# Kernel tuning notes

Measured on AMD Instinct MI355X. Metric: run time of the kernel, lower is better.

Reference implementation:

```python
import jax, jax.numpy as jnp
import numpy as np
import math

B, L, S, T = 16, 128, 128, 128
QDIM, FDIM, HID, ODIM = 512, 512, 512, 512

def setup_inputs() -> dict:
    key = jax.random.key(0)
    ks = jax.random.split(key, 9)
    sc = 0.02
    return {
        "query": jax.random.normal(ks[0], (B, L, QDIM), dtype=jnp.float32),
        "src": jax.random.normal(ks[1], (B, S, FDIM), dtype=jnp.float32),
        "trg": jax.random.normal(ks[2], (B, T, FDIM), dtype=jnp.float32),
        "Wq": jax.random.normal(ks[3], (QDIM, HID), dtype=jnp.float32) * sc,
        "bq": jnp.zeros((HID,), dtype=jnp.float32),
        "Ws": jax.random.normal(ks[4], (FDIM, HID), dtype=jnp.float32) * sc,
        "bs": jnp.zeros((HID,), dtype=jnp.float32),
        "Wo": jax.random.normal(ks[5], (FDIM * 2 + QDIM, ODIM), dtype=jnp.float32) * sc,
        "bo": jnp.zeros((ODIM,), dtype=jnp.float32),
    }

def reference(query, src, trg, Wq, bq, Ws, bs, Wo, bo):
    b, l, _ = query.shape
    s = src.shape[1]
    t = trg.shape[1]
    q = query @ Wq + bq            # [b,l,h]
    s_key = src @ Ws + bs          # [b,s,h]  (src_linear == trg_linear, shared weights)
    t_key = trg @ Ws + bs          # [b,t,h]
    # trilinear scores: [b,l,s,t]
    weight = jnp.einsum('blk,bsk,btk->blst', q, s_key, t_key) / math.sqrt(HID)
    weight = jax.nn.softmax(weight.reshape(b, l, s * t), axis=-1).reshape(b, l, s, t)
    s_ctx = jnp.einsum('blst,bsf->blf', weight, src)
    t_ctx = jnp.einsum('blst,btf->blf', weight, trg)
    x = jnp.concatenate((query, s_ctx, t_ctx), axis=-1)
    return x @ Wo + bo
```

## Files before the change

### kernel.cpp

```cpp
#include <hip/hip_runtime.h>
#include <hip/hip_bf16.h>

typedef __attribute__((ext_vector_type(8))) short short8;
typedef __attribute__((ext_vector_type(4))) short short4v;
typedef __attribute__((ext_vector_type(4))) float f32x4;
typedef __attribute__((ext_vector_type(8))) _Float16 half8;

#define DEVINL static __device__ __forceinline__

constexpr float SCORE_SCALE = 0.063758977414048896f;

typedef const __attribute__((address_space(1))) void gv_t;
typedef __attribute__((address_space(3))) void lv_t;
DEVINL void gload16(const void* g, void* l) {
  __builtin_amdgcn_global_load_lds((gv_t*)g, (lv_t*)l, 16, 0, 0);
}

#define SWZ_ADD(v, pat)                                                    \
  v += __int_as_float(__builtin_amdgcn_ds_swizzle(__float_as_int(v), pat))

template <int M, int N>
DEVINL void gemm16(const _Float16* A, const _Float16* B, int K, int lda, int ldb,
                   _Float16* ldsA, _Float16* ldsB, f32x4 acc[M / 32][N / 32])
{
  const int tid = threadIdx.x, lane = tid & 63;
  const int wr = (tid >> 7) & 1, wc = (tid >> 6) & 1;
  constexpr int MA = M / 32, NB = N / 32;
  int aoff[MA], boff[NB];
#pragma unroll
  for (int i = 0; i < MA; ++i) {
    const int ci = tid + i * 256, row = ci >> 3, c = ci & 7;
    aoff[i] = row * lda + ((c ^ (row & 7)) << 3);
  }
#pragma unroll
  for (int i = 0; i < NB; ++i) {
    const int ci = tid + i * 256, row = ci >> 3, c = ci & 7;
    boff[i] = row * ldb + ((c ^ (row & 7)) << 3);
  }
#define G16STAGE(cur, kk)                                                        \
  {                                                                              \
    _Pragma("unroll")                                                            \
    for (int i = 0; i < MA; ++i)                                                 \
      gload16(A + aoff[i] + (kk), ldsA + (cur) * (M * 64) + (tid + i * 256) * 8);\
    _Pragma("unroll")                                                            \
    for (int i = 0; i < NB; ++i)                                                 \
      gload16(B + boff[i] + (kk), ldsB + (cur) * (N * 64) + (tid + i * 256) * 8);\
  }
  G16STAGE(0, 0);
  __syncthreads();
  for (int kk = 0; kk < K; kk += 64) {
    const int cur = (kk >> 6) & 1;
    if (kk + 64 < K) G16STAGE(cur ^ 1, kk + 64);
    const _Float16* bA = ldsA + cur * (M * 64);
    const _Float16* bB = ldsB + cur * (N * 64);
#pragma unroll
    for (int s = 0; s < 2; ++s) {
      const int cg2 = s * 4 + (lane >> 4);
      half8 afr[MA], bfr[NB];
#pragma unroll
      for (int mi = 0; mi < MA; ++mi) {
        const int r = wr * (M / 2) + mi * 16 + (lane & 15);
        afr[mi] = *(const half8*)(bA + r * 64 + ((cg2 ^ (r & 7)) << 3));
      }
#pragma unroll
      for (int ni = 0; ni < NB; ++ni) {
        const int r = wc * (N / 2) + ni * 16 + (lane & 15);
        bfr[ni] = *(const half8*)(bB + r * 64 + ((cg2 ^ (r & 7)) << 3));
      }
#pragma unroll
      for (int mi = 0; mi < MA; ++mi)
#pragma unroll
        for (int ni = 0; ni < NB; ++ni)
          acc[mi][ni] = __builtin_amdgcn_mfma_f32_16x16x32_f16(afr[mi], bfr[ni], acc[mi][ni], 0, 0, 0);
    }
    __syncthreads();
  }
#undef G16STAGE
}

__global__ __launch_bounds__(256) void k_prep(
    const float* __restrict__ query, const float* __restrict__ src,
    const float* __restrict__ trg,
    const float* __restrict__ Wq, const float* __restrict__ Ws,
    const float* __restrict__ Wo,
    _Float16* __restrict__ x, _Float16* __restrict__ srch,
    _Float16* __restrict__ trgh,
    _Float16* __restrict__ WqT, _Float16* __restrict__ WsT,
    _Float16* __restrict__ WoT,
    _Float16* __restrict__ srcT, _Float16* __restrict__ trgT)
{
  __shared__ float t[32][33];
  const int id = blockIdx.x, tid = threadIdx.x;
  if (id < 1536) {
    const int z = id >> 9;
    const int idx8 = (((id & 511) << 8) + tid) * 8;
    const float* in = (z == 0) ? query : (z == 1) ? src : trg;
    float4 va = *(const float4*)(in + idx8);
    float4 vb = *(const float4*)(in + idx8 + 4);
    half8 h;
    h[0] = (_Float16)va.x; h[1] = (_Float16)va.y;
    h[2] = (_Float16)va.z; h[3] = (_Float16)va.w;
    h[4] = (_Float16)vb.x; h[5] = (_Float16)vb.y;
    h[6] = (_Float16)vb.z; h[7] = (_Float16)vb.w;
    if (z == 0) {
      const int row = idx8 >> 9, col = idx8 & 511;
      *(half8*)(x + (size_t)row * 1536 + col) = h;
    } else {
      _Float16* o = (z == 1) ? srch : trgh;
      *(half8*)(o + idx8) = h;
    }
    return;
  }
  const float* in; _Float16* out; int KK, NN, bx, by; size_t bo = 0;
  if (id < 1792)      { const int u = id - 1536; in = Wq;  out = WqT;  KK = 512;  NN = 512; bx = u & 15; by = u >> 4; }
  else if (id < 2048) { const int u = id - 1792; in = Ws;  out = WsT;  KK = 512;  NN = 512; bx = u & 15; by = u >> 4; }
  else if (id < 2816) { const int u = id - 2048; in = Wo;  out = WoT;  KK = 1536; NN = 512; bx = u & 15; by = u >> 4; }
  else if (id < 3840) { const int u = id - 2816; in = src; out = srcT; KK = 128;  NN = 512; bx = u & 15; by = (u >> 4) & 3; bo = (size_t)(u >> 6) * 65536; }
  else                { const int u = id - 3840; in = trg; out = trgT; KK = 128;  NN = 512; bx = u & 15; by = (u >> 4) & 3; bo = (size_t)(u >> 6) * 65536; }
  const int tx = tid & 31, ty = tid >> 5;
  const int k0 = by * 32, n0 = bx * 32;
#pragma unroll
  for (int i = 0; i < 4; ++i)
    t[ty + i * 8][tx] = in[bo + (size_t)(k0 + ty + i * 8) * NN + n0 + tx];
  __syncthreads();
#pragma unroll
  for (int i = 0; i < 4; ++i)
    out[bo + (size_t)(n0 + ty + i * 8) * KK + k0 + tx] = (_Float16)t[tx][ty + i * 8];
}

__global__ __launch_bounds__(256) void k_proj(
    const _Float16* __restrict__ xq, const _Float16* __restrict__ srch,
    const _Float16* __restrict__ trgh,
    const _Float16* __restrict__ WqT, const _Float16* __restrict__ WsT,
    const float* __restrict__ bq, const float* __restrict__ bs,
    _Float16* __restrict__ qh, _Float16* __restrict__ skh,
    _Float16* __restrict__ tkh)
{
  __shared__ __align__(16) _Float16 lds[24576];
  const int z = blockIdx.z;
  const _Float16* A = (z == 0) ? xq : (z == 1) ? srch : trgh;
  const int lda = (z == 0) ? 1536 : 512;
  const _Float16* BT = (z == 0) ? WqT : WsT;
  const float* bias = (z == 0) ? bq : bs;
  const int brow = blockIdx.y * 64, bcol = blockIdx.x * 128;

  f32x4 acc[2][4] = {};
  gemm16<64, 128>(A + (size_t)brow * lda, BT + (size_t)bcol * 512, 512, lda, 512,
                  lds, lds + 8192, acc);

  const int tid = threadIdx.x, lane = tid & 63;
  const int wr = (tid >> 7) & 1, wc = (tid >> 6) & 1;
  const int r0 = wr * 32 + ((lane >> 4) << 2);
  const int c0 = wc * 64 + (lane & 15);
#pragma unroll
  for (int mi = 0; mi < 2; ++mi)
#pragma unroll
    for (int ni = 0; ni < 4; ++ni) {
      const int col = bcol + c0 + ni * 16;
      const float bv = bias[col];
#pragma unroll
      for (int r = 0; r < 4; ++r) {
        const int row = brow + r0 + mi * 16 + r;
        const float v = acc[mi][ni][r] + bv;
        if (z == 0)      qh[(size_t)row * 512 + col] = (_Float16)(v * SCORE_SCALE);
        else if (z == 1) skh[(size_t)row * 512 + col] = (_Float16)v;
        else             tkh[(size_t)row * 512 + col] = (_Float16)v;
      }
    }
}

__global__ __launch_bounds__(512, 4) void k_score(
    const _Float16* __restrict__ qh, const _Float16* __restrict__ skh,
    const _Float16* __restrict__ tkh,
    _Float16* __restrict__ wct)
{
  __shared__ __align__(16) char pool[67584];
  _Float16* qlds = (_Float16*)(pool + 65536);
  float* wsp   = (float*)(pool);
  float* wtp   = (float*)(pool + 4096);
  float* wfin  = (float*)(pool + 8192);
  float* denom = (float*)(pool + 12288);

  const int raw = blockIdx.x;
  const int swz = (raw & 7) * 128 + (raw >> 3);
  const int b = swz >> 6, l0 = (swz & 63) * 2;

  const int tid = threadIdx.x, lane = tid & 63, wid = tid >> 6;
  const int l = wid >> 2, qs = (wid >> 1) & 1, qt = wid & 1;
  const int cg = lane >> 4;
  const _Float16* skb = skh + (size_t)b * 65536;
  const _Float16* tkb = tkh + (size_t)b * 65536;

  int soff[2];
#pragma unroll
  for (int j = 0; j < 2; ++j) {
    const int ci = j * 512 + tid;
    const int row = ci >> 3, c = ci & 7;
    soff[j] = row * 512 + ((c ^ (row & 7)) << 3);
  }

  if (tid < 256) {
    const int li = tid >> 7, e = (tid & 127) * 4;
    *(short4v*)(qlds + li * 512 + e) =
        *(const short4v*)(qh + (size_t)(b * 128 + l0 + li) * 512 + e);
  }

  const int rbase_s = (qs * 64 + (lane & 15)) * 128;
  const int rbase_t = (qt * 64 + (lane & 15)) * 128;
  const int sw0 = ((0 * 4 + cg) ^ (lane & 7)) << 4;
  const int sw1 = ((1 * 4 + cg) ^ (lane & 7)) << 4;

#define KSTAGE(dst, kk)                                                     \
  {                                                                         \
    char* base_ = pool + (dst) * 32768;                                     \
    _Pragma("unroll")                                                       \
    for (int j = 0; j < 2; ++j) {                                           \
      gload16(skb + soff[j] + (kk), base_ + (j * 512 + tid) * 16);          \
      gload16(tkb + soff[j] + (kk), base_ + 16384 + (j * 512 + tid) * 16);  \
    }                                                                       \
  }

  f32x4 acc[4][4] = {};
  KSTAGE(0, 0);
  __syncthreads();
  int buf = 0;
  for (int it = 0; it < 8; ++it) {
    if (it < 7) KSTAGE(buf ^ 1, (it + 1) * 64);
    const char* S = pool + buf * 32768;
    const char* T = S + 16384;
    const int kk = it * 64;
#pragma unroll
    for (int s = 0; s < 2; ++s) {
      const int swv = s ? sw1 : sw0;
      half8 qv = *(const half8*)(qlds + l * 512 + kk + s * 32 + cg * 8);
      half8 sfr[4], tfr[4];
#pragma unroll
      for (int mi = 0; mi < 4; ++mi)
        sfr[mi] = *(const half8*)(S + rbase_s + mi * 2048 + swv);
#pragma unroll
      for (int ni = 0; ni < 4; ++ni)
        tfr[ni] = *(const half8*)(T + rbase_t + ni * 2048 + swv);
      __builtin_amdgcn_s_setprio(1);
#pragma unroll
      for (int mi = 0; mi < 4; ++mi) {
        half8 a = sfr[mi] * qv;
#pragma unroll
        for (int ni = 0; ni < 4; ++ni)
          acc[mi][ni] = __builtin_amdgcn_mfma_f32_16x16x32_f16(a, tfr[ni], acc[mi][ni], 0, 0, 0);
      }
      __builtin_amdgcn_s_setprio(0);
    }
    __syncthreads();
    buf ^= 1;
  }
#undef KSTAGE

#pragma unroll
  for (int mi = 0; mi < 4; ++mi)
#pragma unroll
    for (int ni = 0; ni < 4; ++ni)
#pragma unroll
      for (int r = 0; r < 4; ++r)
        acc[mi][ni][r] = exp2f(acc[mi][ni][r]);

#pragma unroll
  for (int mi = 0; mi < 4; ++mi)
#pragma unroll
    for (int r = 0; r < 4; ++r) {
      float v = acc[mi][0][r] + acc[mi][1][r] + acc[mi][2][r] + acc[mi][3][r];
      SWZ_ADD(v, 0x041F);
      SWZ_ADD(v, 0x081F);
      SWZ_ADD(v, 0x101F);
      SWZ_ADD(v, 0x201F);
      if ((lane & 15) == 0)
        wsp[(l * 2 + qt) * 128 + qs * 64 + mi * 16 + (lane >> 4) * 4 + r] = v;
    }
#pragma unroll
  for (int ni = 0; ni < 4; ++ni) {
    float v = 0.f;
#pragma unroll
    for (int mi = 0; mi < 4; ++mi)
#pragma unroll
      for (int r = 0; r < 4; ++r) v += acc[mi][ni][r];
    SWZ_ADD(v, 0x401F);
    v += __shfl_xor(v, 32);
    if (lane < 16) wtp[(l * 2 + qs) * 128 + qt * 64 + ni * 16 + lane] = v;
  }
  __syncthreads();

  if (tid < 256) {
    const int li = tid >> 7, idx = tid & 127;
    wfin[(li * 2 + 0) * 128 + idx] =
        wsp[(li * 2 + 0) * 128 + idx] + wsp[(li * 2 + 1) * 128 + idx];
  } else {
    const int u = tid - 256, li = u >> 7, idx = u & 127;
    wfin[(li * 2 + 1) * 128 + idx] =
        wtp[(li * 2 + 0) * 128 + idx] + wtp[(li * 2 + 1) * 128 + idx];
  }
  __syncthreads();
  if (wid < 2) {
    float v = wfin[wid * 256 + lane] + wfin[wid * 256 + lane + 64];
#pragma unroll
    for (int off = 32; off >= 1; off >>= 1) v += __shfl_xor(v, off);
    if (lane == 0) denom[wid] = v;
  }
  __syncthreads();
  const float inv0 = 1.0f / denom[0], inv1 = 1.0f / denom[1];

  if (tid < 256) {
    const int li = tid >> 7, idx = tid & 127;
    const float inv = li ? inv1 : inv0;
    wct[((size_t)(b * 2 + 0) * 128 + l0 + li) * 128 + idx] =
        (_Float16)(wfin[li * 256 + idx] * inv);
  } else {
    const int u = tid - 256, li = u >> 7, idx = u & 127;
    const float inv = li ? inv1 : inv0;
    wct[((size_t)(b * 2 + 1) * 128 + l0 + li) * 128 + idx] =
        (_Float16)(wfin[li * 256 + 128 + idx] * inv);
  }
}

__global__ __launch_bounds__(256) void k_ctx(const _Float16* __restrict__ wct,
                                             const _Float16* __restrict__ srcT,
                                             const _Float16* __restrict__ trgT,
                                             _Float16* __restrict__ x)
{
  __shared__ __align__(16) _Float16 lds[24576];
  const int side = blockIdx.x, fcol = blockIdx.y >> 1, mrow = blockIdx.y & 1;
  const int b = blockIdx.z;
  const _Float16* A  = wct + (size_t)(b * 2 + side) * 16384 + mrow * 64 * 128;
  const _Float16* BT = (side ? trgT : srcT) + (size_t)b * 65536 + fcol * 16384;

  f32x4 acc[2][4] = {};
  gemm16<64, 128>(A, BT, 128, 128, 128, lds, lds + 8192, acc);

  const int tid = threadIdx.x, lane = tid & 63;
  const int wr = (tid >> 7) & 1, wc = (tid >> 6) & 1;
  const int r0 = wr * 32 + ((lane >> 4) << 2);
  const int c0 = wc * 64 + (lane & 15);
  const int xoff = 512 + side * 512 + fcol * 128;
#pragma unroll
  for (int mi = 0; mi < 2; ++mi)
#pragma unroll
    for (int ni = 0; ni < 4; ++ni) {
      const int col = c0 + ni * 16;
#pragma unroll
      for (int r = 0; r < 4; ++r) {
        const int row = mrow * 64 + r0 + mi * 16 + r;
        x[(size_t)(b * 128 + row) * 1536 + xoff + col] = (_Float16)acc[mi][ni][r];
      }
    }
}

__global__ __launch_bounds__(256) void k_out(const _Float16* __restrict__ x,
                                             const _Float16* __restrict__ WoT,
                                             const float* __restrict__ bo,
                                             float* __restrict__ out)
{
  __shared__ __align__(16) _Float16 lds[16384];
  const int brow = blockIdx.y * 64, bcol = blockIdx.x * 64;
  f32x4 acc[2][2] = {};
  gemm16<64, 64>(x + (size_t)brow * 1536, WoT + (size_t)bcol * 1536, 1536, 1536, 1536,
                 lds, lds + 8192, acc);
  const int tid = threadIdx.x, lane = tid & 63;
  const int wr = (tid >> 7) & 1, wc = (tid >> 6) & 1;
  const int r0 = wr * 32 + ((lane >> 4) << 2);
  const int c0 = wc * 32 + (lane & 15);
#pragma unroll
  for (int mi = 0; mi < 2; ++mi)
#pragma unroll
    for (int ni = 0; ni < 2; ++ni) {
      const int col = bcol + c0 + ni * 16;
      const float bv = bo[col];
#pragma unroll
      for (int r = 0; r < 4; ++r) {
        const int row = brow + r0 + mi * 16 + r;
        out[(size_t)row * 512 + col] = acc[mi][ni][r] + bv;
      }
    }
}

extern "C" void kernel_launch(void* const* d_in, const int* in_sizes, int n_in,
                              void* d_out, int out_size, void* d_ws, size_t ws_size,
                              hipStream_t stream)
{
  (void)in_sizes; (void)n_in; (void)out_size; (void)ws_size;
  const float* query = (const float*)d_in[0];
  const float* src   = (const float*)d_in[1];
  const float* trg   = (const float*)d_in[2];
  const float* Wq    = (const float*)d_in[3];
  const float* bq    = (const float*)d_in[4];
  const float* Ws    = (const float*)d_in[5];
  const float* bs    = (const float*)d_in[6];
  const float* Wo    = (const float*)d_in[7];
  const float* bo    = (const float*)d_in[8];
  float* out = (float*)d_out;

  char* w = (char*)d_ws;
  _Float16* x    = (_Float16*)(w);
  _Float16* qh   = (_Float16*)(w + (6u  << 20));
  _Float16* skh  = (_Float16*)(w + (8u  << 20));
  _Float16* tkh  = (_Float16*)(w + (10u << 20));
  _Float16* srch = (_Float16*)(w + (12u << 20));
  _Float16* trgh = (_Float16*)(w + (14u << 20));
  _Float16* WqT  = (_Float16*)(w + (16u << 20));
  _Float16* WsT  = (_Float16*)(w + (16u << 20) + 512 * 512 * 2);
  _Float16* WoT  = (_Float16*)(w + (17u << 20));
  _Float16* srcT = (_Float16*)(w + (19u << 20));
  _Float16* trgT = (_Float16*)(w + (21u << 20));
  _Float16* wct  = (_Float16*)(w + (23u << 20));

  k_prep<<<4864, 256, 0, stream>>>(query, src, trg, Wq, Ws, Wo,
                                   x, srch, trgh, WqT, WsT, WoT, srcT, trgT);
  k_proj<<<dim3(4, 32, 3), 256, 0, stream>>>(x, srch, trgh, WqT, WsT, bq, bs, qh, skh, tkh);
  k_score<<<1024, 512, 0, stream>>>(qh, skh, tkh, wct);
  k_ctx<<<dim3(2, 8, 16), 256, 0, stream>>>(wct, srcT, trgT, x);
  k_out<<<dim3(8, 32), 256, 0, stream>>>(x, WoT, bo, out);
}
```

Before: 79.02 us.

## Load t-key fragments directly from global into registers in score kernel

```diff
diff --git a/kernel.cpp b/kernel.cpp
--- a/kernel.cpp
+++ b/kernel.cpp
@@ -174,8 +174,8 @@
     const _Float16* __restrict__ tkh,
     _Float16* __restrict__ wct)
 {
-  __shared__ __align__(16) char pool[67584];
-  _Float16* qlds = (_Float16*)(pool + 65536);
+  __shared__ __align__(16) char pool[34816];
+  _Float16* qlds = (_Float16*)(pool + 32768);
   float* wsp   = (float*)(pool);
   float* wtp   = (float*)(pool + 4096);
   float* wfin  = (float*)(pool + 8192);
@@ -206,18 +206,26 @@
   }
 
   const int rbase_s = (qs * 64 + (lane & 15)) * 128;
-  const int rbase_t = (qt * 64 + (lane & 15)) * 128;
   const int sw0 = ((0 * 4 + cg) ^ (lane & 7)) << 4;
   const int sw1 = ((1 * 4 + cg) ^ (lane & 7)) << 4;
 
+  int tfo[4];
+#pragma unroll
+  for (int ni = 0; ni < 4; ++ni)
+    tfo[ni] = (qt * 64 + ni * 16 + (lane & 15)) * 512 + cg * 8;
+
+  half8 tf0[4], tf1[4];
+#pragma unroll
+  for (int ni = 0; ni < 4; ++ni) tf0[ni] = *(const half8*)(tkb + tfo[ni]);
+#pragma unroll
+  for (int ni = 0; ni < 4; ++ni) tf1[ni] = *(const half8*)(tkb + tfo[ni] + 32);
+
 #define KSTAGE(dst, kk)                                                     \
   {                                                                         \
-    char* base_ = pool + (dst) * 32768;                                     \
+    char* base_ = pool + (dst) * 16384;                                     \
     _Pragma("unroll")                                                       \
-    for (int j = 0; j < 2; ++j) {                                           \
+    for (int j = 0; j < 2; ++j)                                             \
       gload16(skb + soff[j] + (kk), base_ + (j * 512 + tid) * 16);          \
-      gload16(tkb + soff[j] + (kk), base_ + 16384 + (j * 512 + tid) * 16);  \
-    }                                                                       \
   }
 
   f32x4 acc[4][4] = {};
@@ -225,30 +233,48 @@
   __syncthreads();
   int buf = 0;
   for (int it = 0; it < 8; ++it) {
-    if (it < 7) KSTAGE(buf ^ 1, (it + 1) * 64);
-    const char* S = pool + buf * 32768;
-    const char* T = S + 16384;
     const int kk = it * 64;
-#pragma unroll
-    for (int s = 0; s < 2; ++s) {
-      const int swv = s ? sw1 : sw0;
-      half8 qv = *(const half8*)(qlds + l * 512 + kk + s * 32 + cg * 8);
-      half8 sfr[4], tfr[4];
+    if (it < 7) KSTAGE(buf ^ 1, kk + 64);
+    const char* S = pool + buf * 16384;
+    {
+      half8 qv = *(const half8*)(qlds + l * 512 + kk + cg * 8);
+      half8 sfr[4];
 #pragma unroll
       for (int mi = 0; mi < 4; ++mi)
-        sfr[mi] = *(const half8*)(S + rbase_s + mi * 2048 + swv);
-#pragma unroll
-      for (int ni = 0; ni < 4; ++ni)
-        tfr[ni] = *(const half8*)(T + rbase_t + ni * 2048 + swv);
+        sfr[mi] = *(const half8*)(S + rbase_s + mi * 2048 + sw0);
       __builtin_amdgcn_s_setprio(1);
 #pragma unroll
       for (int mi = 0; mi < 4; ++mi) {
         half8 a = sfr[mi] * qv;
 #pragma unroll
         for (int ni = 0; ni < 4; ++ni)
-          acc[mi][ni] = __builtin_amdgcn_mfma_f32_16x16x32_f16(a, tfr[ni], acc[mi][ni], 0, 0, 0);
+          acc[mi][ni] = __builtin_amdgcn_mfma_f32_16x16x32_f16(a, tf0[ni], acc[mi][ni], 0, 0, 0);
       }
       __builtin_amdgcn_s_setprio(0);
+    }
+    if (it < 7) {
+#pragma unroll
+      for (int ni = 0; ni < 4; ++ni) tf0[ni] = *(const half8*)(tkb + tfo[ni] + kk + 64);
+    }
+    {
+      half8 qv = *(const half8*)(qlds + l * 512 + kk + 32 + cg * 8);
+      half8 sfr[4];
+#pragma unroll
+      for (int mi = 0; mi < 4; ++mi)
+        sfr[mi] = *(const half8*)(S + rbase_s + mi * 2048 + sw1);
+      __builtin_amdgcn_s_setprio(1);
+#pragma unroll
+      for (int mi = 0; mi < 4; ++mi) {
+        half8 a = sfr[mi] * qv;
+#pragma unroll
+        for (int ni = 0; ni < 4; ++ni)
+          acc[mi][ni] = __builtin_amdgcn_mfma_f32_16x16x32_f16(a, tf1[ni], acc[mi][ni], 0, 0, 0);
+      }
+      __builtin_amdgcn_s_setprio(0);
+    }
+    if (it < 7) {
+#pragma unroll
+      for (int ni = 0; ni < 4; ++ni) tf1[ni] = *(const half8*)(tkb + tfo[ni] + kk + 96);
     }
     __syncthreads();
     buf ^= 1;
```

After: 123.0 us. +55.7%, slower.

## Switch score kernel to triple-buffered 32-wide K stages with explicit waitcnt

Applied to the files above, without the earlier changes.

```diff
diff --git a/kernel.cpp b/kernel.cpp
--- a/kernel.cpp
+++ b/kernel.cpp
@@ -174,8 +174,8 @@
     const _Float16* __restrict__ tkh,
     _Float16* __restrict__ wct)
 {
-  __shared__ __align__(16) char pool[67584];
-  _Float16* qlds = (_Float16*)(pool + 65536);
+  __shared__ __align__(16) char pool[51200];
+  _Float16* qlds = (_Float16*)(pool + 49152);
   float* wsp   = (float*)(pool);
   float* wtp   = (float*)(pool + 4096);
   float* wfin  = (float*)(pool + 8192);
@@ -188,15 +188,14 @@
   const int tid = threadIdx.x, lane = tid & 63, wid = tid >> 6;
   const int l = wid >> 2, qs = (wid >> 1) & 1, qt = wid & 1;
   const int cg = lane >> 4;
+  const int ln = lane & 15;
   const _Float16* skb = skh + (size_t)b * 65536;
   const _Float16* tkb = tkh + (size_t)b * 65536;
 
-  int soff[2];
-#pragma unroll
-  for (int j = 0; j < 2; ++j) {
-    const int ci = j * 512 + tid;
-    const int row = ci >> 3, c = ci & 7;
-    soff[j] = row * 512 + ((c ^ (row & 7)) << 3);
+  int soff;
+  {
+    const int row = tid >> 2, c = tid & 3;
+    soff = row * 512 + ((c ^ ((row >> 1) & 3)) << 3);
   }
 
   if (tid < 256) {
@@ -205,53 +204,52 @@
         *(const short4v*)(qh + (size_t)(b * 128 + l0 + li) * 512 + e);
   }
 
-  const int rbase_s = (qs * 64 + (lane & 15)) * 128;
-  const int rbase_t = (qt * 64 + (lane & 15)) * 128;
-  const int sw0 = ((0 * 4 + cg) ^ (lane & 7)) << 4;
-  const int sw1 = ((1 * 4 + cg) ^ (lane & 7)) << 4;
-
-#define KSTAGE(dst, kk)                                                     \
+  const int rbase_s = (qs * 64 + ln) * 64;
+  const int rbase_t = (qt * 64 + ln) * 64;
+  const int sw = (cg ^ ((ln >> 1) & 3)) << 4;
+
+#define KSTAGE(dstbuf, kt)                                                  \
   {                                                                         \
-    char* base_ = pool + (dst) * 32768;                                     \
-    _Pragma("unroll")                                                       \
-    for (int j = 0; j < 2; ++j) {                                           \
-      gload16(skb + soff[j] + (kk), base_ + (j * 512 + tid) * 16);          \
-      gload16(tkb + soff[j] + (kk), base_ + 16384 + (j * 512 + tid) * 16);  \
-    }                                                                       \
+    gload16(skb + soff + (kt) * 32, (dstbuf) + tid * 16);                   \
+    gload16(tkb + soff + (kt) * 32, (dstbuf) + 8192 + tid * 16);            \
   }
 
   f32x4 acc[4][4] = {};
-  KSTAGE(0, 0);
-  __syncthreads();
-  int buf = 0;
-  for (int it = 0; it < 8; ++it) {
-    if (it < 7) KSTAGE(buf ^ 1, (it + 1) * 64);
-    const char* S = pool + buf * 32768;
-    const char* T = S + 16384;
-    const int kk = it * 64;
-#pragma unroll
-    for (int s = 0; s < 2; ++s) {
-      const int swv = s ? sw1 : sw0;
-      half8 qv = *(const half8*)(qlds + l * 512 + kk + s * 32 + cg * 8);
-      half8 sfr[4], tfr[4];
-#pragma unroll
-      for (int mi = 0; mi < 4; ++mi)
-        sfr[mi] = *(const half8*)(S + rbase_s + mi * 2048 + swv);
+  char* bufA = pool;
+  char* bufB = pool + 16384;
+  char* bufC = pool + 32768;
+  KSTAGE(bufA, 0);
+  KSTAGE(bufB, 1);
+  asm volatile("s_waitcnt vmcnt(0) lgkmcnt(0)" ::: "memory");
+  __builtin_amdgcn_sched_barrier(0);
+  __builtin_amdgcn_s_barrier();
+  __builtin_amdgcn_sched_barrier(0);
+
+  for (int it = 0; it < 16; ++it) {
+    if (it < 14) KSTAGE(bufC, it + 2);
+    half8 qv = *(const half8*)(qlds + l * 512 + it * 32 + cg * 8);
+    half8 sfr[4], tfr[4];
+#pragma unroll
+    for (int mi = 0; mi < 4; ++mi)
+      sfr[mi] = *(const half8*)(bufA + rbase_s + mi * 1024 + sw);
+#pragma unroll
+    for (int ni = 0; ni < 4; ++ni)
+      tfr[ni] = *(const half8*)(bufA + 8192 + rbase_t + ni * 1024 + sw);
+    __builtin_amdgcn_s_setprio(1);
+#pragma unroll
+    for (int mi = 0; mi < 4; ++mi) {
+      half8 a = sfr[mi] * qv;
 #pragma unroll
       for (int ni = 0; ni < 4; ++ni)
-        tfr[ni] = *(const half8*)(T + rbase_t + ni * 2048 + swv);
-      __builtin_amdgcn_s_setprio(1);
-#pragma unroll
-      for (int mi = 0; mi < 4; ++mi) {
-        half8 a = sfr[mi] * qv;
-#pragma unroll
-        for (int ni = 0; ni < 4; ++ni)
-          acc[mi][ni] = __builtin_amdgcn_mfma_f32_16x16x32_f16(a, tfr[ni], acc[mi][ni], 0, 0, 0);
-      }
-      __builtin_amdgcn_s_setprio(0);
-    }
-    __syncthreads();
-    buf ^= 1;
+        acc[mi][ni] = __builtin_amdgcn_mfma_f32_16x16x32_f16(a, tfr[ni], acc[mi][ni], 0, 0, 0);
+    }
+    __builtin_amdgcn_s_setprio(0);
+    if (it < 14) { asm volatile("s_waitcnt vmcnt(2)" ::: "memory"); }
+    else         { asm volatile("s_waitcnt vmcnt(0)" ::: "memory"); }
+    __builtin_amdgcn_sched_barrier(0);
+    __builtin_amdgcn_s_barrier();
+    __builtin_amdgcn_sched_barrier(0);
+    char* t_ = bufA; bufA = bufB; bufB = bufC; bufC = t_;
   }
 #undef KSTAGE
 
```

Measured after the change: 79.52 us. About the same (+0.6%).
